# Kernel optimization log

Measured on AMD Instinct MI355X. Metric: run time of the kernel, lower is better.

Reference implementation:

```python
import jax, jax.numpy as jnp
import numpy as np

S, B, D, H, MLP_H, W = 2048, 4, 1024, 16, 4096, 16
EPS = 1e-6

def _ln(x):
    m = jnp.mean(x, axis=-1, keepdims=True)
    v = jnp.var(x, axis=-1, keepdims=True)
    return (x - m) / jnp.sqrt(v + EPS)

def setup_inputs() -> dict:
    key = jax.random.key(0)
    ks = jax.random.split(key, 12)
    sc = lambda k, shape, fan: jax.random.normal(k, shape, jnp.float32) / np.sqrt(fan)
    return {
        'x': jax.random.normal(ks[0], (S, B, D), jnp.float32),
        'c': jax.random.normal(ks[1], (B, D), jnp.float32),
        'ada_w': sc(ks[2], (6 * D, D), D),
        'ada_b': jax.random.normal(ks[3], (6 * D,), jnp.float32) * 0.02,
        'in_proj_w': sc(ks[4], (3 * D, D), D),
        'in_proj_b': jax.random.normal(ks[5], (3 * D,), jnp.float32) * 0.02,
        'out_proj_w': sc(ks[6], (D, D), D),
        'out_proj_b': jax.random.normal(ks[7], (D,), jnp.float32) * 0.02,
        'mlp_w1': sc(ks[8], (MLP_H, D), D),
        'mlp_b1': jax.random.normal(ks[9], (MLP_H,), jnp.float32) * 0.02,
        'mlp_w2': sc(ks[10], (D, MLP_H), MLP_H),
        'mlp_b2': jax.random.normal(ks[11], (D,), jnp.float32) * 0.02,
        'num_heads': H,
        'window_size': W,
    }

def _attn(x, in_proj_w, in_proj_b, out_proj_w, out_proj_b, num_heads, window_size):
    s, b, d = x.shape
    dh = d // num_heads
    qkv = x @ in_proj_w.T + in_proj_b            # [S,B,3D]
    q, k, v = jnp.split(qkv, 3, axis=-1)
    def heads(t):  # [S,B,D] -> [B,H,S,dh]
        return t.reshape(s, b, num_heads, dh).transpose(1, 2, 0, 3)
    q, k, v = heads(q), heads(k), heads(v)
    scores = jnp.einsum('bhsd,bhtd->bhst', q, k) / np.sqrt(dh)
    idx = jnp.arange(s)
    band = jnp.abs(idx[:, None] - idx[None, :]) <= window_size  # [S,S]
    scores = jnp.where(band[None, None], scores, -jnp.inf)
    attn = jax.nn.softmax(scores, axis=-1)
    o = jnp.einsum('bhst,bhtd->bhsd', attn, v)   # [B,H,S,dh]
    o = o.transpose(2, 0, 1, 3).reshape(s, b, d)
    return o @ out_proj_w.T + out_proj_b

def reference(x, c, ada_w, ada_b, in_proj_w, in_proj_b, out_proj_w, out_proj_b, mlp_w1, mlp_b1, mlp_w2, mlp_b2, num_heads, window_size):
    mod = jax.nn.relu(c) @ ada_w.T + ada_b       # [B,6D]
    sh_msa, sc_msa, g_msa, sh_mlp, sc_mlp, g_mlp = jnp.split(mod, 6, axis=1)
    xm = _ln(x) * (1.0 + sc_msa[None]) + sh_msa[None]
    x = x + g_msa[None] * _attn(xm, in_proj_w, in_proj_b, out_proj_w, out_proj_b, num_heads, window_size)
    xm = _ln(x) * (1.0 + sc_mlp[None]) + sh_mlp[None]
    h = jax.nn.relu(xm @ mlp_w1.T + mlp_b1)
    mlp_out = h @ mlp_w2.T + mlp_b2
    return x + g_mlp[None] * mlp_out
```

## Files before the change

kernel.cpp:

```cpp
#include <hip/hip_runtime.h>

#define S_LEN 2048
#define BATCH 4
#define DMODEL 1024
#define NHEAD 16
#define MROWS (S_LEN * BATCH)
#define MOD6 (6 * DMODEL)

typedef float f32x4 __attribute__((ext_vector_type(4)));
typedef short bf16x8 __attribute__((ext_vector_type(8)));
typedef unsigned short ushort_t;

__device__ __forceinline__ unsigned short f2bf(float f) {
  unsigned u = __float_as_uint(f);
  u += 0x7FFF + ((u >> 16) & 1);
  return (unsigned short)(u >> 16);
}
__device__ __forceinline__ float bf2f(unsigned short h) {
  return __uint_as_float(((unsigned)h) << 16);
}
__device__ __forceinline__ float wave_sum(float v) {
#pragma unroll
  for (int off = 32; off > 0; off >>= 1) v += __shfl_xor(v, off, 64);
  return v;
}
__device__ __forceinline__ void mfma16(f32x4& c, bf16x8 a, bf16x8 b) {
  asm volatile("v_mfma_f32_16x16x32_bf16 %0, %1, %2, %0" : "+v"(c) : "v"(a), "v"(b));
}
__device__ __forceinline__ void mfma_fence() {
  __builtin_amdgcn_sched_barrier(0);
  asm volatile("s_nop 7\n\ts_nop 7\n\ts_nop 7");
  __builtin_amdgcn_sched_barrier(0);
}
__device__ __forceinline__ void async16(const void* g, void* l) {
  __builtin_amdgcn_global_load_lds((const __attribute__((address_space(1))) void*)g,
                                   (__attribute__((address_space(3))) void*)l, 16, 0, 0);
}

__launch_bounds__(256)
__global__ void castk(const float4* __restrict__ in, ushort4* __restrict__ out, int n4) {
  int i = blockIdx.x * 256 + threadIdx.x;
  if (i < n4) {
    float4 v = in[i];
    ushort4 o;
    o.x = f2bf(v.x); o.y = f2bf(v.y); o.z = f2bf(v.z); o.w = f2bf(v.w);
    out[i] = o;
  }
}

__launch_bounds__(256)
__global__ void ada_k(const float* __restrict__ c, const float* __restrict__ aw,
                      const float* __restrict__ ab, float* __restrict__ mod) {
  int j = blockIdx.x;
  int b = threadIdx.x >> 6;
  int l = threadIdx.x & 63;
  const float* wrow = aw + (size_t)j * DMODEL;
  const float* crow = c + b * DMODEL;
  float s = 0.f;
#pragma unroll 4
  for (int i = l; i < DMODEL; i += 64) {
    float cv = crow[i];
    cv = cv > 0.f ? cv : 0.f;
    s += cv * wrow[i];
  }
  s = wave_sum(s);
  if (l == 0) mod[b * MOD6 + j] = s + ab[j];
}

__launch_bounds__(256)
__global__ void ln_mod(const float* __restrict__ x, const float* __restrict__ mod,
                       int sh_off, int sc_off, ushort_t* __restrict__ out) {
  __shared__ float red[8];
  int row = blockIdx.x;
  int b = row & 3;
  int tid = threadIdx.x;
  const float4* xr = (const float4*)(x + (size_t)row * DMODEL);
  float4 v = xr[tid];
  float s = v.x + v.y + v.z + v.w;
  float s2 = v.x * v.x + v.y * v.y + v.z * v.z + v.w * v.w;
  s = wave_sum(s);
  s2 = wave_sum(s2);
  int w = tid >> 6, l = tid & 63;
  if (l == 0) { red[w] = s; red[4 + w] = s2; }
  __syncthreads();
  s = red[0] + red[1] + red[2] + red[3];
  s2 = red[4] + red[5] + red[6] + red[7];
  float mean = s * (1.0f / DMODEL);
  float var = s2 * (1.0f / DMODEL) - mean * mean;
  float inv = rsqrtf(var + 1e-6f);
  const float* shp = mod + b * MOD6 + sh_off;
  const float* scp = mod + b * MOD6 + sc_off;
  float vv[4] = {v.x, v.y, v.z, v.w};
  ushort4 ov;
  ushort_t* op = (ushort_t*)&ov;
#pragma unroll
  for (int j = 0; j < 4; j++) {
    int idx = tid * 4 + j;
    float y = (vv[j] - mean) * inv * (1.0f + scp[idx]) + shp[idx];
    op[j] = f2bf(y);
  }
  ((ushort4*)(out + (size_t)row * DMODEL))[tid] = ov;
}

__launch_bounds__(256)
__global__ void attn_mfma(const ushort_t* __restrict__ qkv, ushort_t* __restrict__ out) {
  const int l = threadIdx.x & 63;
  const int widx = blockIdx.x * 4 + (threadIdx.x >> 6);
  const int qblk = widx & 63;
  const int bh = widx >> 6;
  const int h = bh & 15;
  const int b = bh >> 4;
  const int q0 = qblk * 32;
  int k0 = q0 - 16;
  if (k0 < 0) k0 = 0;
  if (k0 > S_LEN - 64) k0 = S_LEN - 64;
  const int lr = l & 15;
  const int g = l >> 4;

  const char* base = (const char*)qkv;

  bf16x8 qf[2][2], kf[4][2];
#pragma unroll
  for (int nt = 0; nt < 2; nt++) {
    size_t rowb = (size_t)((q0 + 16 * nt + lr) * 4 + b) * 6144 + h * 128 + 16 * g;
#pragma unroll
    for (int ks = 0; ks < 2; ks++)
      qf[nt][ks] = *(const bf16x8*)(base + rowb + 64 * ks);
  }
#pragma unroll
  for (int mt = 0; mt < 4; mt++) {
    size_t rowb = (size_t)((k0 + 16 * mt + lr) * 4 + b) * 6144 + 2048 + h * 128 + 16 * g;
#pragma unroll
    for (int ks = 0; ks < 2; ks++)
      kf[mt][ks] = *(const bf16x8*)(base + rowb + 64 * ks);
  }

  f32x4 acc[4][2] = {};
  __builtin_amdgcn_s_setprio(1);
#pragma unroll
  for (int mt = 0; mt < 4; mt++)
#pragma unroll
    for (int nt = 0; nt < 2; nt++)
#pragma unroll
      for (int ks = 0; ks < 2; ks++)
        mfma16(acc[mt][nt], kf[mt][ks], qf[nt][ks]);
  __builtin_amdgcn_s_setprio(0);
  mfma_fence();

  float p0[16], p1[16];
  const int sq0 = q0 + lr, sq1 = q0 + 16 + lr;
  float m0 = -1e30f, m1 = -1e30f;
#pragma unroll
  for (int mt = 0; mt < 4; mt++)
#pragma unroll
    for (int i = 0; i < 4; i++) {
      int sk = k0 + 16 * mt + 4 * g + i;
      int d0 = sq0 - sk, d1 = sq1 - sk;
      float s0 = (d0 <= 16 && d0 >= -16) ? acc[mt][0][i] * 0.125f : -1e30f;
      float s1 = (d1 <= 16 && d1 >= -16) ? acc[mt][1][i] * 0.125f : -1e30f;
      p0[mt * 4 + i] = s0;
      p1[mt * 4 + i] = s1;
      m0 = fmaxf(m0, s0);
      m1 = fmaxf(m1, s1);
    }
  m0 = fmaxf(m0, __shfl_xor(m0, 16, 64));
  m0 = fmaxf(m0, __shfl_xor(m0, 32, 64));
  m1 = fmaxf(m1, __shfl_xor(m1, 16, 64));
  m1 = fmaxf(m1, __shfl_xor(m1, 32, 64));
  float l0 = 0.f, l1 = 0.f;
#pragma unroll
  for (int j = 0; j < 16; j++) {
    float e0 = __expf(p0[j] - m0);
    float e1 = __expf(p1[j] - m1);
    p0[j] = e0; p1[j] = e1;
    l0 += e0; l1 += e1;
  }
  l0 += __shfl_xor(l0, 16, 64); l0 += __shfl_xor(l0, 32, 64);
  l1 += __shfl_xor(l1, 16, 64); l1 += __shfl_xor(l1, 32, 64);
  const float inv0 = 1.0f / l0, inv1 = 1.0f / l1;

  const size_t vb = (size_t)b * 6144 + 4096 + h * 128;
  for (int c = 0; c < 8; c++) {
    float o0[8] = {}, o1[8] = {};
#pragma unroll
    for (int mt = 0; mt < 4; mt++)
#pragma unroll
      for (int i = 0; i < 4; i++) {
        int t = k0 + 16 * mt + 4 * g + i;
        bf16x8 v = *(const bf16x8*)(base + (size_t)t * 24576 + vb + 16 * c);
        float pa = p0[mt * 4 + i], pb = p1[mt * 4 + i];
#pragma unroll
        for (int d = 0; d < 8; d++) {
          float vf = bf2f((unsigned short)v[d]);
          o0[d] += pa * vf;
          o1[d] += pb * vf;
        }
      }
#pragma unroll
    for (int d = 0; d < 8; d++) {
      o0[d] += __shfl_xor(o0[d], 16, 64); o0[d] += __shfl_xor(o0[d], 32, 64);
      o1[d] += __shfl_xor(o1[d], 16, 64); o1[d] += __shfl_xor(o1[d], 32, 64);
    }
    if (g < 2) {
      int sq = q0 + 16 * g + lr;
      bf16x8 ov;
#pragma unroll
      for (int d = 0; d < 8; d++) {
        float val = (g ? o1[d] : o0[d]) * (g ? inv1 : inv0);
        ov[d] = (short)f2bf(val);
      }
      *(bf16x8*)((char*)out + (size_t)(sq * 4 + b) * 2048 + h * 128 + c * 16) = ov;
    }
  }
}

template <int EPI, int K>
__launch_bounds__(256, 2)
__global__ void gemm_bt(const ushort_t* __restrict__ A, const ushort_t* __restrict__ W,
                        const float* __restrict__ bias, const float* __restrict__ res,
                        const float* __restrict__ gmod, void* __restrict__ outp,
                        int M, int N) {
  __shared__ alignas(16) ushort_t As[2][128 * 64];
  __shared__ alignas(16) ushort_t Bs[2][128 * 64];
  const int tid = threadIdx.x;
  const int w = tid >> 6;
  const int l = tid & 63;

  int bx = blockIdx.x, by = blockIdx.y;
  {
    const int nbx = gridDim.x;
    const int nwg = nbx * gridDim.y;
    if ((nwg & 7) == 0) {
      int lin = by * nbx + bx;
      int nlin = (lin & 7) * (nwg >> 3) + (lin >> 3);
      bx = nlin % nbx;
      by = nlin / nbx;
    }
  }
  const int row0 = by * 128;
  const int col0 = bx * 128;
  const int wr = (w >> 1) * 64;
  const int wc = (w & 1) * 64;

  f32x4 acc[4][4] = {};

  const int srow = tid >> 3;
  const int scc = (((tid & 7) ^ (srow & 7)) << 3);
  const ushort_t* ga = A + (size_t)(row0 + srow) * K + scc;
  const ushort_t* gb = W + (size_t)(col0 + srow) * K + scc;
  const int ldst = w * 1024;

  const int lrow = l & 15;
  const int g = l >> 4;
  const int cx0 = ((g ^ (lrow & 7)) << 4);
  const int cx1 = (((4 + g) ^ (lrow & 7)) << 4);
  const int arow = (wr + lrow) * 128;
  const int brow = (wc + lrow) * 128;

  const int nk = K >> 6;
  {
    char* lA = (char*)As[0] + ldst;
    char* lB = (char*)Bs[0] + ldst;
#pragma unroll
    for (int r = 0; r < 4; r++) async16(ga + (size_t)(32 * r) * K, lA + r * 4096);
#pragma unroll
    for (int r = 0; r < 4; r++) async16(gb + (size_t)(32 * r) * K, lB + r * 4096);
    ga += 64;
    gb += 64;
  }
  int cur = 0;
  for (int it = 0; it < nk; ++it) {
    if (it + 1 < nk) {
      char* lA = (char*)As[cur ^ 1] + ldst;
      char* lB = (char*)Bs[cur ^ 1] + ldst;
#pragma unroll
      for (int r = 0; r < 4; r++) async16(ga + (size_t)(32 * r) * K, lA + r * 4096);
#pragma unroll
      for (int r = 0; r < 4; r++) async16(gb + (size_t)(32 * r) * K, lB + r * 4096);
      ga += 64;
      gb += 64;
      asm volatile("s_waitcnt vmcnt(8)" ::: "memory");
    } else {
      asm volatile("s_waitcnt vmcnt(0)" ::: "memory");
    }
    __builtin_amdgcn_sched_barrier(0);
    __builtin_amdgcn_s_barrier();
    __builtin_amdgcn_sched_barrier(0);
    const char* Ab = (const char*)As[cur];
    const char* Bb = (const char*)Bs[cur];
#pragma unroll
    for (int kk = 0; kk < 2; kk++) {
      const int cx = kk ? cx1 : cx0;
      bf16x8 afr[4], bfr[4];
#pragma unroll
      for (int m = 0; m < 4; m++) afr[m] = *(const bf16x8*)(Ab + arow + m * 2048 + cx);
#pragma unroll
      for (int n = 0; n < 4; n++) bfr[n] = *(const bf16x8*)(Bb + brow + n * 2048 + cx);
      __builtin_amdgcn_s_setprio(1);
#pragma unroll
      for (int m = 0; m < 4; m++)
#pragma unroll
        for (int n = 0; n < 4; n++) mfma16(acc[m][n], afr[m], bfr[n]);
      __builtin_amdgcn_s_setprio(0);
    }
    __builtin_amdgcn_sched_barrier(0);
    __builtin_amdgcn_s_barrier();
    __builtin_amdgcn_sched_barrier(0);
    cur ^= 1;
  }
  mfma_fence();

  const int crow = row0 + wr + g * 4;
  const int ccol = col0 + wc + lrow;
#pragma unroll
  for (int m = 0; m < 4; m++) {
#pragma unroll
    for (int i = 0; i < 4; i++) {
      int grow = crow + m * 16 + i;
#pragma unroll
      for (int n = 0; n < 4; n++) {
        int gcol = ccol + n * 16;
        float v = acc[m][n][i] + bias[gcol];
        if constexpr (EPI == 0) {
          ((ushort_t*)outp)[(size_t)grow * N + gcol] = f2bf(v);
        } else if constexpr (EPI == 1) {
          ((ushort_t*)outp)[(size_t)grow * N + gcol] = f2bf(v > 0.f ? v : 0.f);
        } else {
          int bb = grow & 3;
          ((float*)outp)[(size_t)grow * N + gcol] =
              res[(size_t)grow * N + gcol] + gmod[bb * MOD6 + gcol] * v;
        }
      }
    }
  }
}

extern "C" void kernel_launch(void* const* d_in, const int* in_sizes, int n_in,
                              void* d_out, int out_size, void* d_ws, size_t ws_size,
                              hipStream_t stream) {
  const float* x     = (const float*)d_in[0];
  const float* c     = (const float*)d_in[1];
  const float* ada_w = (const float*)d_in[2];
  const float* ada_b = (const float*)d_in[3];
  const float* in_w  = (const float*)d_in[4];
  const float* in_b  = (const float*)d_in[5];
  const float* out_w = (const float*)d_in[6];
  const float* out_b = (const float*)d_in[7];
  const float* w1    = (const float*)d_in[8];
  const float* b1    = (const float*)d_in[9];
  const float* w2    = (const float*)d_in[10];
  const float* b2    = (const float*)d_in[11];

  char* ws = (char*)d_ws;
  float* mod    = (float*)ws;
  ushort_t* wq  = (ushort_t*)(ws + 98304);
  ushort_t* wo  = (ushort_t*)(ws + 6389760);
  ushort_t* wm1 = (ushort_t*)(ws + 8486912);
  ushort_t* wm2 = (ushort_t*)(ws + 16875520);
  ushort_t* xm  = (ushort_t*)(ws + 25264128);
  ushort_t* qkv = (ushort_t*)(ws + 42041344);
  ushort_t* att = (ushort_t*)(ws + 92372992);
  ushort_t* h   = (ushort_t*)(ws + 42041344);
  float* x1 = (float*)d_out;

  castk<<<(3072 * 1024 / 4 + 255) / 256, 256, 0, stream>>>((const float4*)in_w, (ushort4*)wq, 3072 * 1024 / 4);
  castk<<<(1024 * 1024 / 4 + 255) / 256, 256, 0, stream>>>((const float4*)out_w, (ushort4*)wo, 1024 * 1024 / 4);
  castk<<<(4096 * 1024 / 4 + 255) / 256, 256, 0, stream>>>((const float4*)w1, (ushort4*)wm1, 4096 * 1024 / 4);
  castk<<<(1024 * 4096 / 4 + 255) / 256, 256, 0, stream>>>((const float4*)w2, (ushort4*)wm2, 1024 * 4096 / 4);

  ada_k<<<MOD6, 256, 0, stream>>>(c, ada_w, ada_b, mod);

  ln_mod<<<MROWS, 256, 0, stream>>>(x, mod, 0, 1024, xm);
  gemm_bt<0, 1024><<<dim3(3072 / 128, MROWS / 128), 256, 0, stream>>>(xm, wq, in_b, nullptr, nullptr, qkv, MROWS, 3072);
  attn_mfma<<<(BATCH * NHEAD * (S_LEN / 32)) / 4, 256, 0, stream>>>(qkv, att);
  gemm_bt<2, 1024><<<dim3(1024 / 128, MROWS / 128), 256, 0, stream>>>(att, wo, out_b, x, mod + 2 * DMODEL, x1, MROWS, 1024);
  ln_mod<<<MROWS, 256, 0, stream>>>(x1, mod, 3 * DMODEL, 4 * DMODEL, xm);
  gemm_bt<1, 1024><<<dim3(4096 / 128, MROWS / 128), 256, 0, stream>>>(xm, wm1, b1, nullptr, nullptr, h, MROWS, 4096);
  gemm_bt<2, 4096><<<dim3(1024 / 128, MROWS / 128), 256, 0, stream>>>(h, wm2, b2, x1, mod + 5 * DMODEL, (float*)d_out, MROWS, 1024);
}
```

Measured before the change: 334.6 us.

## Use 8-wave 256xBN GEMM tiles with prefetch interleaved into MFMA phases

```diff
diff --git a/kernel.cpp b/kernel.cpp
--- a/kernel.cpp
+++ b/kernel.cpp
@@ -214,17 +214,20 @@
   }
 }
 
-template <int EPI, int K>
-__launch_bounds__(256, 2)
-__global__ void gemm_bt(const ushort_t* __restrict__ A, const ushort_t* __restrict__ W,
-                        const float* __restrict__ bias, const float* __restrict__ res,
-                        const float* __restrict__ gmod, void* __restrict__ outp,
-                        int M, int N) {
-  __shared__ alignas(16) ushort_t As[2][128 * 64];
-  __shared__ alignas(16) ushort_t Bs[2][128 * 64];
+template <int EPI, int K, int BN>
+__launch_bounds__(512, 1)
+__global__ void gemm8(const ushort_t* __restrict__ A, const ushort_t* __restrict__ W,
+                      const float* __restrict__ bias, const float* __restrict__ res,
+                      const float* __restrict__ gmod, void* __restrict__ outp,
+                      int M, int N) {
+  constexpr int NT = BN / 64;
+  __shared__ alignas(16) ushort_t As[2][256 * 64];
+  __shared__ alignas(16) ushort_t Bs[2][BN * 64];
   const int tid = threadIdx.x;
   const int w = tid >> 6;
   const int l = tid & 63;
+  const int wr = w >> 2;
+  const int wn = w & 3;
 
   int bx = blockIdx.x, by = blockIdx.y;
   {
@@ -237,12 +240,10 @@
       by = nlin / nbx;
     }
   }
-  const int row0 = by * 128;
-  const int col0 = bx * 128;
-  const int wr = (w >> 1) * 64;
-  const int wc = (w & 1) * 64;
-
-  f32x4 acc[4][4] = {};
+  const int row0 = by * 256;
+  const int col0 = bx * BN;
+
+  f32x4 acc[8][NT] = {};
 
   const int srow = tid >> 3;
   const int scc = (((tid & 7) ^ (srow & 7)) << 3);
@@ -254,71 +255,83 @@
   const int g = l >> 4;
   const int cx0 = ((g ^ (lrow & 7)) << 4);
   const int cx1 = (((4 + g) ^ (lrow & 7)) << 4);
-  const int arow = (wr + lrow) * 128;
-  const int brow = (wc + lrow) * 128;
+  const int abase = (wr * 128 + lrow) * 128;
+  const int bbase = (wn * (BN / 4) + lrow) * 128;
 
   const int nk = K >> 6;
   {
     char* lA = (char*)As[0] + ldst;
     char* lB = (char*)Bs[0] + ldst;
 #pragma unroll
-    for (int r = 0; r < 4; r++) async16(ga + (size_t)(32 * r) * K, lA + r * 4096);
-#pragma unroll
-    for (int r = 0; r < 4; r++) async16(gb + (size_t)(32 * r) * K, lB + r * 4096);
+    for (int r = 0; r < 4; r++) async16(ga + (size_t)(64 * r) * K, lA + r * 8192);
+#pragma unroll
+    for (int r = 0; r < NT; r++) async16(gb + (size_t)(64 * r) * K, lB + r * 8192);
     ga += 64;
     gb += 64;
   }
   int cur = 0;
   for (int it = 0; it < nk; ++it) {
-    if (it + 1 < nk) {
-      char* lA = (char*)As[cur ^ 1] + ldst;
-      char* lB = (char*)Bs[cur ^ 1] + ldst;
-#pragma unroll
-      for (int r = 0; r < 4; r++) async16(ga + (size_t)(32 * r) * K, lA + r * 4096);
-#pragma unroll
-      for (int r = 0; r < 4; r++) async16(gb + (size_t)(32 * r) * K, lB + r * 4096);
-      ga += 64;
-      gb += 64;
-      asm volatile("s_waitcnt vmcnt(8)" ::: "memory");
-    } else {
-      asm volatile("s_waitcnt vmcnt(0)" ::: "memory");
-    }
+    asm volatile("s_waitcnt vmcnt(0)" ::: "memory");
     __builtin_amdgcn_sched_barrier(0);
     __builtin_amdgcn_s_barrier();
     __builtin_amdgcn_sched_barrier(0);
+    const bool pf = (it + 1 < nk);
+    char* lA = (char*)As[cur ^ 1] + ldst;
+    char* lB = (char*)Bs[cur ^ 1] + ldst;
     const char* Ab = (const char*)As[cur];
     const char* Bb = (const char*)Bs[cur];
-#pragma unroll
-    for (int kk = 0; kk < 2; kk++) {
+    bf16x8 bfr[2][NT];
+#pragma unroll
+    for (int ph = 0; ph < 4; ph++) {
+      const int qm = ph >> 1, kk = ph & 1;
+      if (pf) {
+        if (ph == 0) {
+          async16(ga, lA);
+          async16(ga + (size_t)64 * K, lA + 8192);
+        } else if (ph == 1) {
+          async16(ga + (size_t)128 * K, lA + 16384);
+          async16(ga + (size_t)192 * K, lA + 24576);
+        } else if (ph == 2) {
+          async16(gb, lB);
+          async16(gb + (size_t)64 * K, lB + 8192);
+        } else if constexpr (NT == 4) {
+          async16(gb + (size_t)128 * K, lB + 16384);
+          async16(gb + (size_t)192 * K, lB + 24576);
+        }
+      }
       const int cx = kk ? cx1 : cx0;
-      bf16x8 afr[4], bfr[4];
-#pragma unroll
-      for (int m = 0; m < 4; m++) afr[m] = *(const bf16x8*)(Ab + arow + m * 2048 + cx);
-#pragma unroll
-      for (int n = 0; n < 4; n++) bfr[n] = *(const bf16x8*)(Bb + brow + n * 2048 + cx);
+      if (qm == 0) {
+#pragma unroll
+        for (int n = 0; n < NT; n++)
+          bfr[kk][n] = *(const bf16x8*)(Bb + bbase + n * 2048 + cx);
+      }
+      bf16x8 afr[4];
+#pragma unroll
+      for (int m = 0; m < 4; m++)
+        afr[m] = *(const bf16x8*)(Ab + abase + (qm * 4 + m) * 2048 + cx);
       __builtin_amdgcn_s_setprio(1);
 #pragma unroll
       for (int m = 0; m < 4; m++)
 #pragma unroll
-        for (int n = 0; n < 4; n++) mfma16(acc[m][n], afr[m], bfr[n]);
+        for (int n = 0; n < NT; n++)
+          mfma16(acc[qm * 4 + m][n], afr[m], bfr[kk][n]);
       __builtin_amdgcn_s_setprio(0);
     }
-    __builtin_amdgcn_sched_barrier(0);
-    __builtin_amdgcn_s_barrier();
-    __builtin_amdgcn_sched_barrier(0);
+    ga += 64;
+    gb += 64;
     cur ^= 1;
   }
   mfma_fence();
 
-  const int crow = row0 + wr + g * 4;
-  const int ccol = col0 + wc + lrow;
-#pragma unroll
-  for (int m = 0; m < 4; m++) {
+  const int crow = row0 + wr * 128 + g * 4;
+  const int ccol = col0 + wn * (BN / 4) + lrow;
+#pragma unroll
+  for (int m = 0; m < 8; m++) {
 #pragma unroll
     for (int i = 0; i < 4; i++) {
       int grow = crow + m * 16 + i;
 #pragma unroll
-      for (int n = 0; n < 4; n++) {
+      for (int n = 0; n < NT; n++) {
         int gcol = ccol + n * 16;
         float v = acc[m][n][i] + bias[gcol];
         if constexpr (EPI == 0) {
@@ -371,10 +384,10 @@
   ada_k<<<MOD6, 256, 0, stream>>>(c, ada_w, ada_b, mod);
 
   ln_mod<<<MROWS, 256, 0, stream>>>(x, mod, 0, 1024, xm);
-  gemm_bt<0, 1024><<<dim3(3072 / 128, MROWS / 128), 256, 0, stream>>>(xm, wq, in_b, nullptr, nullptr, qkv, MROWS, 3072);
+  gemm8<0, 1024, 256><<<dim3(3072 / 256, MROWS / 256), 512, 0, stream>>>(xm, wq, in_b, nullptr, nullptr, qkv, MROWS, 3072);
   attn_mfma<<<(BATCH * NHEAD * (S_LEN / 32)) / 4, 256, 0, stream>>>(qkv, att);
-  gemm_bt<2, 1024><<<dim3(1024 / 128, MROWS / 128), 256, 0, stream>>>(att, wo, out_b, x, mod + 2 * DMODEL, x1, MROWS, 1024);
+  gemm8<2, 1024, 128><<<dim3(1024 / 128, MROWS / 256), 512, 0, stream>>>(att, wo, out_b, x, mod + 2 * DMODEL, x1, MROWS, 1024);
   ln_mod<<<MROWS, 256, 0, stream>>>(x1, mod, 3 * DMODEL, 4 * DMODEL, xm);
-  gemm_bt<1, 1024><<<dim3(4096 / 128, MROWS / 128), 256, 0, stream>>>(xm, wm1, b1, nullptr, nullptr, h, MROWS, 4096);
-  gemm_bt<2, 4096><<<dim3(1024 / 128, MROWS / 128), 256, 0, stream>>>(h, wm2, b2, x1, mod + 5 * DMODEL, (float*)d_out, MROWS, 1024);
-}
+  gemm8<1, 1024, 256><<<dim3(4096 / 256, MROWS / 256), 512, 0, stream>>>(xm, wm1, b1, nullptr, nullptr, h, MROWS, 4096);
+  gemm8<2, 4096, 128><<<dim3(1024 / 128, MROWS / 256), 512, 0, stream>>>(h, wm2, b2, x1, mod + 5 * DMODEL, (float*)d_out, MROWS, 1024);
+}
```

After: 395.2 us. 18.1% more time.
